# Kernel optimization log

Measured on AMD Instinct MI355X. Metric: run time of the kernel, lower is better.

The kernel has to match this reference:

```python
import jax, jax.numpy as jnp
import numpy as np

# ConvMem dims
B, Cx, Cy, L, K, S, N = 64, 16, 64, 32, 5, 1, 1024
M = (L - K) // S + 1  # 28
DT, TAU_X, TAU_Y = 0.1, 1.0, 0.1
ETA_X, ETA_Y = DT / TAU_X, DT / TAU_Y
MAX_STEPS = 50


def setup_inputs() -> dict:
    key = jax.random.key(0)
    k1, k2, k3, k4 = jax.random.split(key, 4)
    x0 = jax.random.normal(k1, (B, Cx, L, L), dtype=jnp.float32)
    f0 = jax.random.uniform(k2, (B, Cy, M, M), dtype=jnp.float32) / 100.0
    # Conv2d weight (shared between conv and convT), shape (Cy, Cx, K, K)
    w_conv = jax.random.normal(k3, (Cy, Cx, K, K), dtype=jnp.float32) / np.sqrt(Cx * K * K).astype(np.float32)
    # W: (N, Cy*M*M), kaiming_normal fan_in init
    W = jax.random.normal(k4, (N, Cy * M * M), dtype=jnp.float32) * np.sqrt(2.0 / (Cy * M * M)).astype(np.float32)
    return {"x0": x0, "f0": f0, "w_conv": w_conv, "W": W}


def _conv(x, w):
    # PyTorch Conv2d(Cx, Cy, K, S, bias=False), valid padding
    return jax.lax.conv_general_dilated(x, w, (S, S), 'VALID',
                                        dimension_numbers=('NCHW', 'OIHW', 'NCHW'))


def _convT(f, w):
    # PyTorch ConvTranspose2d with the *same* weight as conv (adjoint of _conv)
    return jax.lax.conv_transpose(f, w, (S, S), 'VALID',
                                  dimension_numbers=('NCHW', 'OIHW', 'NCHW'),
                                  transpose_kernel=True)


def reference(x0, f0, w_conv, W):
    def step(carry, _):
        x_prev, f_prev = carry
        # fc: z = W @ flatten(f_prev);  g = softmax(z) over N (dim=1, beta=1)
        z = jnp.einsum('nk,bk->bn', W, f_prev.reshape(B, Cy * M * M))  # (B, N)
        g = jax.nn.softmax(z, axis=1)
        # fcT: y = W^T @ g, reshaped to (B, Cy, M, M)
        y = (g @ W).reshape(B, Cy, M, M)
        # f nonlin: softmax over channel dim (dim=1)
        f_new = jax.nn.softmax(y + _conv(x_prev, w_conv), axis=1)
        x_new = _convT(f_prev, w_conv)
        f = (1.0 - ETA_Y) * f_prev + ETA_Y * f_new
        x = (1.0 - ETA_X) * x_prev + ETA_X * x_new
        return (x, f), None

    (x, f), _ = jax.lax.scan(step, (x0, f0), None, length=MAX_STEPS)
    return x, f
```

## Files before the change

kernel.cpp:

```cpp
#include <hip/hip_runtime.h>

#define BB 64
#define CXC 16
#define CYC 64
#define LL 32
#define MM 28
#define NN 1024
#define SP 784
#define KTOT 50176
#define NSTEPS 50
#define NSPLIT 49

using short8  = __attribute__((ext_vector_type(8))) short;
using floatx4 = __attribute__((ext_vector_type(4))) float;

typedef __attribute__((address_space(1))) unsigned int gu32;
typedef __attribute__((address_space(3))) unsigned int su32;

__device__ __forceinline__ ushort f2b(float v) {
    union { float f; unsigned u; } a; a.f = v;
    unsigned r = a.u + 0x7fff + ((a.u >> 16) & 1);
    return (ushort)(r >> 16);
}
__device__ __forceinline__ unsigned pk2(float a, float b) {
    return (unsigned)f2b(a) | ((unsigned)f2b(b) << 16);
}
__device__ __forceinline__ float b2f(ushort u) {
    union { unsigned u; float f; } a; a.u = ((unsigned)u) << 16; return a.f;
}

__device__ __forceinline__ unsigned char f2e4(float v) {
    const unsigned u = __float_as_uint(v);
    const unsigned s = (u >> 24) & 0x80;
    float a = fabsf(v);
    if (a >= 448.f) return (unsigned char)(s | 0x7E);
    if (a < 0.015625f) {
        int q = (int)rintf(a * 512.f);
        return (unsigned char)(s | (unsigned)q);
    }
    unsigned au = u & 0x7fffffffu;
    unsigned r = au + 0xFFFFFu + ((au >> 20) & 1u);
    int exp = (int)(r >> 23) - 127;
    if (exp > 8) return (unsigned char)(s | 0x7E);
    unsigned mant = (r >> 20) & 7u;
    return (unsigned char)(s | (((unsigned)(exp + 7)) << 3) | mant);
}

#define WSC 256.0f
#define FSC 64.0f
#define GSC 256.0f
#define ZDESC (1.0f / (WSC * FSC))
#define YDESC (1.0f / (WSC * GSC))

__global__ __launch_bounds__(256) void wconvert_kernel(const float* __restrict__ W,
                                                       unsigned char* __restrict__ Wb8,
                                                       unsigned char* __restrict__ WT8) {
    __shared__ float t[32][33];
    const int k0 = blockIdx.x * 32, n0 = blockIdx.y * 32;
    const int tid = threadIdx.x, r = tid >> 5, c = tid & 31;
#pragma unroll
    for (int p = 0; p < 4; p++) {
        const int rr = r + p * 8;
        t[rr][c] = W[(size_t)(n0 + rr) * KTOT + k0 + c];
    }
    __syncthreads();
    const int rw = tid >> 3, c4 = (tid & 7) * 4;
#if __has_builtin(__builtin_amdgcn_cvt_pk_fp8_f32)
    unsigned u1 = 0, u2 = 0;
    u1 = __builtin_amdgcn_cvt_pk_fp8_f32(t[rw][c4 + 0] * WSC, t[rw][c4 + 1] * WSC, u1, false);
    u1 = __builtin_amdgcn_cvt_pk_fp8_f32(t[rw][c4 + 2] * WSC, t[rw][c4 + 3] * WSC, u1, true);
    *(unsigned*)&Wb8[(size_t)(n0 + rw) * KTOT + k0 + c4] = u1;
    u2 = __builtin_amdgcn_cvt_pk_fp8_f32(t[c4 + 0][rw] * WSC, t[c4 + 1][rw] * WSC, u2, false);
    u2 = __builtin_amdgcn_cvt_pk_fp8_f32(t[c4 + 2][rw] * WSC, t[c4 + 3][rw] * WSC, u2, true);
    *(unsigned*)&WT8[(size_t)(k0 + rw) * NN + n0 + c4] = u2;
#else
    uchar4 o1, o2;
    o1.x = f2e4(t[rw][c4 + 0] * WSC); o1.y = f2e4(t[rw][c4 + 1] * WSC);
    o1.z = f2e4(t[rw][c4 + 2] * WSC); o1.w = f2e4(t[rw][c4 + 3] * WSC);
    *(uchar4*)&Wb8[(size_t)(n0 + rw) * KTOT + k0 + c4] = o1;
    o2.x = f2e4(t[c4 + 0][rw] * WSC); o2.y = f2e4(t[c4 + 1][rw] * WSC);
    o2.z = f2e4(t[c4 + 2][rw] * WSC); o2.w = f2e4(t[c4 + 3][rw] * WSC);
    *(uchar4*)&WT8[(size_t)(k0 + rw) * NN + n0 + c4] = o2;
#endif
}

__global__ __launch_bounds__(256) void cvt_f0_kernel(const float* __restrict__ f,
                                                     unsigned char* __restrict__ o) {
    const size_t i = ((size_t)blockIdx.x * 256 + threadIdx.x) * 4;
    const float4 v = *(const float4*)(f + i);
    uchar4 pk;
    pk.x = f2e4(v.x * FSC); pk.y = f2e4(v.y * FSC);
    pk.z = f2e4(v.z * FSC); pk.w = f2e4(v.w * FSC);
    *(uchar4*)(o + i) = pk;
}

__global__ __launch_bounds__(256) void wbuild_kernel(const float* __restrict__ wc,
                                                     ushort* __restrict__ wcA,
                                                     ushort* __restrict__ wcT) {
    const int bid = blockIdx.x, tid = threadIdx.x;
    if (bid < 64) {
        const int cy = bid;
        for (int k = tid; k < 416; k += 256) {
            const int tap = k >> 4, cx = k & 15;
            const float v = (tap < 25) ? wc[cy * 400 + cx * 25 + tap] : 0.f;
            wcA[cy * 416 + k] = f2b(v);
        }
    } else {
        const int cx = bid - 64;
        for (int k = tid; k < 1600; k += 256) {
            const int tap = k >> 6, cy = k & 63;
            wcT[cx * 1600 + k] = f2b(wc[cy * 400 + cx * 25 + tap]);
        }
    }
}

__global__ __launch_bounds__(256) void init_x_kernel(const float* __restrict__ x0,
                                                     float* __restrict__ xcl,
                                                     ushort* __restrict__ x16) {
    const int b = blockIdx.x, tid = threadIdx.x;
    __shared__ float xs[16384];
    for (int c = tid; c < 4096; c += 256)
        ((float4*)xs)[c] = ((const float4*)(x0 + (size_t)b * 16384))[c];
    __syncthreads();
    for (int p = tid; p < 1024; p += 256) {
        float v[16];
#pragma unroll
        for (int cx = 0; cx < 16; cx++) v[cx] = xs[cx * 1024 + p];
        float* dst = xcl + ((size_t)b * 1024 + p) * 16;
#pragma unroll
        for (int q = 0; q < 4; q++)
            *(float4*)(dst + q * 4) = make_float4(v[q*4], v[q*4+1], v[q*4+2], v[q*4+3]);
        uint4 u0, u1;
        u0.x = pk2(v[0], v[1]);  u0.y = pk2(v[2], v[3]);
        u0.z = pk2(v[4], v[5]);  u0.w = pk2(v[6], v[7]);
        u1.x = pk2(v[8], v[9]);  u1.y = pk2(v[10], v[11]);
        u1.z = pk2(v[12], v[13]); u1.w = pk2(v[14], v[15]);
        ushort* d16 = x16 + ((size_t)b * 1024 + p) * 16;
        *(uint4*)d16 = u0; *(uint4*)(d16 + 8) = u1;
    }
}

__global__ __launch_bounds__(256) void final_x_kernel(const float* __restrict__ xcl,
                                                      float* __restrict__ dout) {
    const int b = blockIdx.x, tid = threadIdx.x;
    __shared__ float xs[16384];
    for (int c = tid; c < 4096; c += 256)
        ((float4*)xs)[c] = ((const float4*)(xcl + (size_t)b * 16384))[c];
    __syncthreads();
    for (int idx = tid; idx < 16384; idx += 256) {
        const int cx = idx >> 10, p = idx & 1023;
        dout[(size_t)b * 16384 + idx] = xs[p * 16 + cx];
    }
}

__global__ __launch_bounds__(256) void init_fpad_kernel(const float* __restrict__ f0,
                                                        ushort* __restrict__ fpad) {
    const int b = blockIdx.x, rg = blockIdx.y;
    const int tid = threadIdx.x;
    __shared__ float fs[64 * 112];
    const float* src = f0 + (size_t)b * KTOT + rg * 112;
    for (int c = tid; c < 1792; c += 256) {
        const int cy = c / 28, p4 = (c % 28) * 4;
        *(float4*)&fs[cy * 112 + p4] = *(const float4*)(src + (size_t)cy * SP + p4);
    }
    __syncthreads();
    for (int c = tid; c < 896; c += 256) {
        const int pl = c >> 3, g8 = (c & 7) * 8;
        union { ushort u[8]; uint4 v; } pk;
#pragma unroll
        for (int e = 0; e < 8; e++) pk.u[e] = f2b(fs[(g8 + e) * 112 + pl]);
        const int pos = rg * 112 + pl, i = pos / 28, j = pos % 28;
        *(uint4*)(fpad + (((size_t)b * 36 + 4 + i) * 36 + 4 + j) * 64 + g8) = pk.v;
    }
}

__global__ __launch_bounds__(256, 3) void gemm1_kernel(const unsigned char* __restrict__ A,
                                                       const unsigned char* __restrict__ B,
                                                       float* __restrict__ C) {
    const int bx = blockIdx.x, by = blockIdx.y;
    const int tid = threadIdx.x, l = tid & 63, w = tid >> 6;
    const int wr = w >> 1, wc = w & 1;
    const int lr = l & 15, lg = l >> 4;
    const int sw = (lr >> 1) & 3;
    const int hi8 = (lg & 1) * 8;
    __shared__ __attribute__((aligned(16))) unsigned char As[2][4096];
    __shared__ __attribute__((aligned(16))) unsigned char Bs[2][8192];

    floatx4 acc[2][4];
#pragma unroll
    for (int mi = 0; mi < 2; mi++)
#pragma unroll
        for (int ni = 0; ni < 4; ni++) acc[mi][ni] = (floatx4){0.f, 0.f, 0.f, 0.f};

    const size_t kbase = (size_t)by * 1024;

    auto STAGE = [&](int buf, int kc) {
        const size_t koff = kbase + (size_t)kc * 64;
        {
            const int row = tid >> 2;
            const int kk = (((tid & 3) ^ ((row >> 1) & 3)) << 4);
            __builtin_amdgcn_global_load_lds((gu32*)(A + (size_t)row * KTOT + koff + kk),
                                             (su32*)&As[buf][tid * 16], 16, 0, 0);
        }
#pragma unroll
        for (int i = 0; i < 2; i++) {
            const int q = i * 256 + tid;
            const int rl = q >> 2;
            const int kk = (((q & 3) ^ ((rl >> 1) & 3)) << 4);
            const int row = bx * 128 + rl;
            __builtin_amdgcn_global_load_lds((gu32*)(B + (size_t)row * KTOT + koff + kk),
                                             (su32*)&Bs[buf][q * 16], 16, 0, 0);
        }
    };

    STAGE(0, 0);
#pragma unroll 1
    for (int kc = 0; kc < 16; kc++) {
        const int cur = kc & 1;
        if (kc < 15) {
            STAGE(cur ^ 1, kc + 1);
            asm volatile("s_waitcnt vmcnt(3)" ::: "memory");
        } else {
            asm volatile("s_waitcnt vmcnt(0)" ::: "memory");
        }
        __builtin_amdgcn_s_barrier();
#pragma unroll
        for (int kb = 0; kb < 2; kb++) {
            const int co = (((kb * 2 + (lg >> 1)) ^ sw) << 4) + hi8;
            long a[2];
#pragma unroll
            for (int mi = 0; mi < 2; mi++)
                a[mi] = *(const long*)&As[cur][(wr * 32 + mi * 16 + lr) * 64 + co];
#pragma unroll
            for (int ni = 0; ni < 4; ni++) {
                const long b = *(const long*)&Bs[cur][(wc * 64 + ni * 16 + lr) * 64 + co];
                acc[0][ni] = __builtin_amdgcn_mfma_f32_16x16x32_fp8_fp8(a[0], b, acc[0][ni], 0, 0, 0);
                acc[1][ni] = __builtin_amdgcn_mfma_f32_16x16x32_fp8_fp8(a[1], b, acc[1][ni], 0, 0, 0);
            }
        }
        __builtin_amdgcn_s_barrier();
    }
    float* cp = C + (size_t)by * (BB * NN) + (size_t)(wr * 32 + ((l >> 4) << 2)) * NN
              + bx * 128 + wc * 64 + (l & 15);
#pragma unroll
    for (int mi = 0; mi < 2; mi++)
#pragma unroll
        for (int ni = 0; ni < 4; ni++)
#pragma unroll
            for (int q = 0; q < 4; q++)
                cp[(size_t)(mi * 16 + q) * NN + ni * 16] = acc[mi][ni][q];
}

__global__ __launch_bounds__(1024) void softmax_g_kernel(const float* __restrict__ zpart,
                                                         unsigned char* __restrict__ g8) {
    const int b = blockIdx.x, tid = threadIdx.x;
    float s = 0.f;
#pragma unroll 7
    for (int sp = 0; sp < NSPLIT; sp++) s += zpart[(size_t)sp * (BB * NN) + b * NN + tid];
    s *= ZDESC;
    __shared__ float red[32];
    float m = s;
#pragma unroll
    for (int off = 32; off > 0; off >>= 1) m = fmaxf(m, __shfl_down(m, off));
    if ((tid & 63) == 0) red[tid >> 6] = m;
    __syncthreads();
    float bm = red[0];
#pragma unroll
    for (int e = 1; e < 16; e++) bm = fmaxf(bm, red[e]);
    const float ev = __expf(s - bm);
    float ssum = ev;
#pragma unroll
    for (int off = 32; off > 0; off >>= 1) ssum += __shfl_down(ssum, off);
    __syncthreads();
    if ((tid & 63) == 0) red[16 + (tid >> 6)] = ssum;
    __syncthreads();
    float tot = red[16];
#pragma unroll
    for (int e = 1; e < 16; e++) tot += red[16 + e];
    g8[b * NN + tid] = f2e4(ev * (GSC / tot));
}

__global__ __launch_bounds__(256, 3) void gemm2_convT_kernel(const unsigned char* __restrict__ A,
                                                             const unsigned char* __restrict__ B,
                                                             float* __restrict__ C,
                                                             const ushort* __restrict__ fpad,
                                                             const ushort* __restrict__ wcT,
                                                             const float* __restrict__ xin,
                                                             float* __restrict__ xout,
                                                             ushort* __restrict__ x16o) {
    __shared__ __attribute__((aligned(16))) unsigned char As[2][4096];
    __shared__ __attribute__((aligned(16))) unsigned char Bs[2][8192];
    const int tid = threadIdx.x, l = tid & 63, w = tid >> 6;
    const int lr = l & 15, lg = l >> 4;

    if (blockIdx.x < 256) {
        const int sub = blockIdx.x, b = sub & 63, pg = sub >> 6;
        floatx4 acc[4];
#pragma unroll
        for (int n = 0; n < 4; n++) acc[n] = (floatx4){0.f, 0.f, 0.f, 0.f};
        int p[4], p1[4], p2[4];
#pragma unroll
        for (int n = 0; n < 4; n++) {
            p[n]  = pg * 256 + (w * 4 + n) * 16 + lr;
            p1[n] = p[n] >> 5;
            p2[n] = p[n] & 31;
        }
        const ushort* fb_b = fpad + (size_t)b * (36 * 36 * 64);
        const int cy_lo = lg * 8;

        for (int s = 0; s < 50; s++) {
            const short8 af = *(const short8*)(wcT + (size_t)lr * 1600 + s * 32 + lg * 8);
            const int tap = s >> 1;
            const int ky = tap / 5, kx = tap % 5;
            const int cy_lane = ((s & 1) << 5) + cy_lo;
            short8 bf[4];
#pragma unroll
            for (int n = 0; n < 4; n++) {
                const size_t ad = (((size_t)(p1[n] + 4 - ky)) * 36 + (p2[n] + 4 - kx)) * 64 + cy_lane;
                bf[n] = *(const short8*)(fb_b + ad);
            }
#pragma unroll
            for (int n = 0; n < 4; n++)
                acc[n] = __builtin_amdgcn_mfma_f32_16x16x32_bf16(af, bf[n], acc[n], 0, 0, 0);
        }
#pragma unroll
        for (int n = 0; n < 4; n++) {
            const size_t base = ((size_t)b * 1024 + p[n]) * 16 + lg * 4;
            const float4 xo = *(const float4*)(xin + base);
            float4 r;
            r.x = 0.9f * xo.x + 0.1f * acc[n][0];
            r.y = 0.9f * xo.y + 0.1f * acc[n][1];
            r.z = 0.9f * xo.z + 0.1f * acc[n][2];
            r.w = 0.9f * xo.w + 0.1f * acc[n][3];
            *(float4*)(xout + base) = r;
            uint2 pk; pk.x = pk2(r.x, r.y); pk.y = pk2(r.z, r.w);
            *(uint2*)(x16o + base) = pk;
        }
        return;
    }

    const int bx = blockIdx.x - 256;
    const int wr = w >> 1, wc = w & 1;
    const int sw = (lr >> 1) & 3;
    const int hi8 = (lg & 1) * 8;

    floatx4 acc[2][4];
#pragma unroll
    for (int mi = 0; mi < 2; mi++)
#pragma unroll
        for (int ni = 0; ni < 4; ni++) acc[mi][ni] = (floatx4){0.f, 0.f, 0.f, 0.f};

    auto STAGE = [&](int buf, int kc) {
        const size_t koff = (size_t)kc * 64;
        {
            const int row = tid >> 2;
            const int kk = (((tid & 3) ^ ((row >> 1) & 3)) << 4);
            __builtin_amdgcn_global_load_lds((gu32*)(A + (size_t)row * NN + koff + kk),
                                             (su32*)&As[buf][tid * 16], 16, 0, 0);
        }
#pragma unroll
        for (int i = 0; i < 2; i++) {
            const int q = i * 256 + tid;
            const int rl = q >> 2;
            const int kk = (((q & 3) ^ ((rl >> 1) & 3)) << 4);
            const int row = bx * 128 + rl;
            __builtin_amdgcn_global_load_lds((gu32*)(B + (size_t)row * NN + koff + kk),
                                             (su32*)&Bs[buf][q * 16], 16, 0, 0);
        }
    };

    STAGE(0, 0);
#pragma unroll 1
    for (int kc = 0; kc < 16; kc++) {
        const int cur = kc & 1;
        if (kc < 15) {
            STAGE(cur ^ 1, kc + 1);
            asm volatile("s_waitcnt vmcnt(3)" ::: "memory");
        } else {
            asm volatile("s_waitcnt vmcnt(0)" ::: "memory");
        }
        __builtin_amdgcn_s_barrier();
#pragma unroll
        for (int kb = 0; kb < 2; kb++) {
            const int co = (((kb * 2 + (lg >> 1)) ^ sw) << 4) + hi8;
            long a[2];
#pragma unroll
            for (int mi = 0; mi < 2; mi++)
                a[mi] = *(const long*)&As[cur][(wr * 32 + mi * 16 + lr) * 64 + co];
#pragma unroll
            for (int ni = 0; ni < 4; ni++) {
                const long b = *(const long*)&Bs[cur][(wc * 64 + ni * 16 + lr) * 64 + co];
                acc[0][ni] = __builtin_amdgcn_mfma_f32_16x16x32_fp8_fp8(a[0], b, acc[0][ni], 0, 0, 0);
                acc[1][ni] = __builtin_amdgcn_mfma_f32_16x16x32_fp8_fp8(a[1], b, acc[1][ni], 0, 0, 0);
            }
        }
        __builtin_amdgcn_s_barrier();
    }
    float* cp = C + (size_t)(wr * 32 + ((l >> 4) << 2)) * KTOT
              + bx * 128 + wc * 64 + (l & 15);
#pragma unroll
    for (int mi = 0; mi < 2; mi++)
#pragma unroll
        for (int ni = 0; ni < 4; ni++)
#pragma unroll
            for (int q = 0; q < 4; q++)
                cp[(size_t)(mi * 16 + q) * KTOT + ni * 16] = acc[mi][ni][q];
}

__global__ __launch_bounds__(256) void conv_mfma_kernel(const ushort* __restrict__ x16,
                                                        const ushort* __restrict__ wcA,
                                                        const float* __restrict__ y,
                                                        ushort* __restrict__ fpad,
                                                        unsigned char* __restrict__ f8std,
                                                        float* __restrict__ f32o,
                                                        const int write_f) {
    const int b = blockIdx.x, rg = blockIdx.y;
    const int tid = threadIdx.x, l = tid & 63, w = tid >> 6;
    const int lr = l & 15, lg = l >> 4;
    __shared__ float yt[64 * 196];
    ushort* ft = (ushort*)yt;

    {
        const float* yb = y + (size_t)b * KTOT + rg * 196;
        for (int c = tid; c < 3136; c += 256) {
            const int cy = c / 49, p4 = (c % 49) * 4;
            float4 v = *(const float4*)(yb + (size_t)cy * SP + p4);
            v.x *= YDESC; v.y *= YDESC; v.z *= YDESC; v.w *= YDESC;
            *(float4*)&yt[cy * 196 + p4] = v;
        }
    }

    const int nf = (w == 0) ? 4 : 3;
    const int fb = (w == 0) ? 0 : (1 + 3 * w);

    floatx4 acc[4][4];
#pragma unroll
    for (int m = 0; m < 4; m++)
#pragma unroll
        for (int n = 0; n < 4; n++) acc[m][n] = (floatx4){0.f, 0.f, 0.f, 0.f};

    int pos_l[4], ii[4], jj[4];
#pragma unroll
    for (int n = 0; n < 4; n++) {
        int pl = (fb + n) * 16 + lr;
        if (pl > 195) pl = 195;
        pos_l[n] = pl;
        ii[n] = rg * 7 + pl / 28;
        jj[n] = pl % 28;
    }

    const int t_lane = lg >> 1;
    const int cx0 = (lg & 1) * 8;
    const ushort* xb = x16 + ((size_t)b << 14);

    for (int s = 0; s < 13; s++) {
        short8 af[4];
#pragma unroll
        for (int m = 0; m < 4; m++)
            af[m] = *(const short8*)(wcA + (size_t)(m * 16 + lr) * 416 + s * 32 + lg * 8);
        const int tap = 2 * s + t_lane;
        const int ky = tap / 5, kx = tap % 5;
        short8 bf[4];
#pragma unroll
        for (int n = 0; n < 4; n++) {
            if (n < nf) {
                const int pp = (ii[n] + ky) * 32 + (jj[n] + kx);
                bf[n] = *(const short8*)(xb + (size_t)pp * 16 + cx0);
            }
        }
#pragma unroll
        for (int n = 0; n < 4; n++) {
            if (n < nf) {
#pragma unroll
                for (int m = 0; m < 4; m++)
                    acc[m][n] = __builtin_amdgcn_mfma_f32_16x16x32_bf16(af[m], bf[n], acc[m][n], 0, 0, 0);
            }
        }
    }
    __syncthreads();

#pragma unroll
    for (int n = 0; n < 4; n++) {
        if (n < nf) {
            float v[16];
#pragma unroll
            for (int m = 0; m < 4; m++)
#pragma unroll
                for (int q = 0; q < 4; q++) {
                    const int cy = m * 16 + lg * 4 + q;
                    v[m * 4 + q] = acc[m][n][q] + yt[cy * 196 + pos_l[n]];
                }
            float mx = v[0];
#pragma unroll
            for (int e = 1; e < 16; e++) mx = fmaxf(mx, v[e]);
            mx = fmaxf(mx, __shfl_xor(mx, 16));
            mx = fmaxf(mx, __shfl_xor(mx, 32));
            float ss = 0.f;
#pragma unroll
            for (int e = 0; e < 16; e++) { v[e] = __expf(v[e] - mx); ss += v[e]; }
            ss += __shfl_xor(ss, 16);
            ss += __shfl_xor(ss, 32);
            const float inv = 1.0f / ss;
            const bool valid = (((fb + n) * 16 + lr) < 196) && write_f;
            float* fo = f32o + (size_t)b * KTOT + rg * 196 + pos_l[n];
#pragma unroll
            for (int m = 0; m < 4; m++)
#pragma unroll
                for (int q = 0; q < 4; q++) {
                    const int cy = m * 16 + lg * 4 + q;
                    const float fv = v[m * 4 + q] * inv;
                    acc[m][n][q] = fv;
                    if (valid) fo[(size_t)cy * SP] = fv;
                }
        }
    }
    __syncthreads();

#pragma unroll
    for (int n = 0; n < 4; n++) {
        if (n < nf) {
#pragma unroll
            for (int m = 0; m < 4; m++)
#pragma unroll
                for (int q = 0; q < 4; q++)
                    ft[pos_l[n] * 72 + m * 16 + lg * 4 + q] = f2b(acc[m][n][q]);
        }
    }
    __syncthreads();

    for (int c = tid; c < 196 * 4; c += 256) {
        const int pl = c >> 2, ch = (c & 3) * 16;
        const uint4 v0 = *(const uint4*)&ft[pl * 72 + ch];
        const uint4 v1 = *(const uint4*)&ft[pl * 72 + ch + 8];
        const int gi = rg * 7 + pl / 28, gj = pl % 28;
        ushort* dst = fpad + (((size_t)b * 36 + 4 + gi) * 36 + 4 + gj) * 64 + ch;
        *(uint4*)dst = v0; *(uint4*)(dst + 8) = v1;
    }
    for (int c = tid; c < 1600; c += 256) {
        const int cy = c & 63, p8 = (c >> 6) * 8;
        if (p8 < 196) {
            union { unsigned char u[8]; unsigned w[2]; } pk;
#pragma unroll
            for (int e = 0; e < 8; e++)
                pk.u[e] = f2e4(b2f(ft[(p8 + e) * 72 + cy]) * FSC);
            unsigned* dst = (unsigned*)(f8std + (size_t)b * KTOT + (size_t)cy * SP + rg * 196 + p8);
            dst[0] = pk.w[0];
            if (p8 <= 188) dst[1] = pk.w[1];
        }
    }
}

extern "C" void kernel_launch(void* const* d_in, const int* in_sizes, int n_in,
                              void* d_out, int out_size, void* d_ws, size_t ws_size,
                              hipStream_t stream) {
    const float* x0    = (const float*)d_in[0];
    const float* f0    = (const float*)d_in[1];
    const float* wconv = (const float*)d_in[2];
    const float* W     = (const float*)d_in[3];

    const size_t XSZ = (size_t)BB * CXC * LL * LL;
    const size_t FSZ = (size_t)BB * KTOT;

    char* pp = (char*)d_ws;
    unsigned char* Wb8  = (unsigned char*)pp; pp += (size_t)NN * KTOT;
    unsigned char* WT8  = (unsigned char*)pp; pp += (size_t)NN * KTOT;
    float*  xcl0  = (float*)pp;  pp += (size_t)BB * 1024 * 16 * 4;
    float*  xcl1  = (float*)pp;  pp += (size_t)BB * 1024 * 16 * 4;
    ushort* x16a  = (ushort*)pp; pp += (size_t)BB * 1024 * 16 * 2;
    ushort* x16b  = (ushort*)pp; pp += (size_t)BB * 1024 * 16 * 2;
    pp += 4096;
    ushort* fpad  = (ushort*)pp; pp += (size_t)BB * 36 * 36 * 64 * 2;
    unsigned char* f8std = (unsigned char*)pp; pp += FSZ;
    float*  zy    = (float*)pp;  pp += (size_t)NSPLIT * BB * NN * 4;
    unsigned char* g8 = (unsigned char*)pp; pp += (size_t)BB * NN;
    ushort* wcA   = (ushort*)pp; pp += (size_t)64 * 416 * 2;
    ushort* wcT   = (ushort*)pp; pp += (size_t)16 * 1600 * 2;

    float*  xcl[2] = {xcl0, xcl1};
    ushort* x16[2] = {x16a, x16b};
    float*  f32o = (float*)d_out + XSZ;

    hipMemsetAsync(fpad, 0, (size_t)BB * 36 * 36 * 64 * 2, stream);
    hipMemsetAsync(x16a, 0, (size_t)BB * 1024 * 16 * 2 * 2 + 4096, stream);

    wconvert_kernel<<<dim3(KTOT / 32, NN / 32), 256, 0, stream>>>(W, Wb8, WT8);
    wbuild_kernel<<<80, 256, 0, stream>>>(wconv, wcA, wcT);
    init_x_kernel<<<64, 256, 0, stream>>>(x0, xcl0, x16a);
    cvt_f0_kernel<<<(int)(FSZ / 1024), 256, 0, stream>>>(f0, f8std);
    init_fpad_kernel<<<dim3(64, 7), 256, 0, stream>>>(f0, fpad);

    for (int t = 0; t < NSTEPS; t++) {
        const int cur = t & 1, nxt = cur ^ 1;
        gemm1_kernel<<<dim3(8, NSPLIT), 256, 0, stream>>>(f8std, Wb8, zy);
        softmax_g_kernel<<<BB, 1024, 0, stream>>>(zy, g8);
        gemm2_convT_kernel<<<256 + KTOT / 128, 256, 0, stream>>>(
            g8, WT8, zy, fpad, wcT, xcl[cur], xcl[nxt], x16[nxt]);
        conv_mfma_kernel<<<dim3(64, 4), 256, 0, stream>>>(x16[cur], wcA, zy, fpad, f8std, f32o,
                                                          t == NSTEPS - 1 ? 1 : 0);
    }
    final_x_kernel<<<64, 256, 0, stream>>>(xcl[0], (float*)d_out);
}
```

Measured before the change: 4.338 ms.

## Triple-buffer GEMM LDS stages and widen W conversion tiles

Both fp8 GEMM kernels move from double to triple LDS buffering. This lets the trailing barrier in each k-iteration be dropped, since a buffer is only overwritten two stages later. The W fp8 conversion/transpose kernel now uses 64x64 tiles with float4 loads and 16-byte packed stores instead of 32x32 tiles with scalar traffic. The cost is more LDS per block (36KB instead of 24KB), which may reduce occupancy. Removing the barrier also depends on the single remaining barrier being enough to order reads against later async writes.

```diff
diff --git a/kernel.cpp b/kernel.cpp
--- a/kernel.cpp
+++ b/kernel.cpp
@@ -46,6 +46,18 @@
     return (unsigned char)(s | (((unsigned)(exp + 7)) << 3) | mant);
 }
 
+__device__ __forceinline__ unsigned pk4e4(float a, float b, float c, float d) {
+#if __has_builtin(__builtin_amdgcn_cvt_pk_fp8_f32)
+    unsigned u = 0;
+    u = __builtin_amdgcn_cvt_pk_fp8_f32(a, b, u, false);
+    u = __builtin_amdgcn_cvt_pk_fp8_f32(c, d, u, true);
+    return u;
+#else
+    return (unsigned)f2e4(a) | ((unsigned)f2e4(b) << 8)
+         | ((unsigned)f2e4(c) << 16) | ((unsigned)f2e4(d) << 24);
+#endif
+}
+
 #define WSC 256.0f
 #define FSC 64.0f
 #define GSC 256.0f
@@ -55,33 +67,34 @@
 __global__ __launch_bounds__(256) void wconvert_kernel(const float* __restrict__ W,
                                                        unsigned char* __restrict__ Wb8,
                                                        unsigned char* __restrict__ WT8) {
-    __shared__ float t[32][33];
-    const int k0 = blockIdx.x * 32, n0 = blockIdx.y * 32;
-    const int tid = threadIdx.x, r = tid >> 5, c = tid & 31;
-#pragma unroll
-    for (int p = 0; p < 4; p++) {
-        const int rr = r + p * 8;
-        t[rr][c] = W[(size_t)(n0 + rr) * KTOT + k0 + c];
-    }
-    __syncthreads();
-    const int rw = tid >> 3, c4 = (tid & 7) * 4;
-#if __has_builtin(__builtin_amdgcn_cvt_pk_fp8_f32)
-    unsigned u1 = 0, u2 = 0;
-    u1 = __builtin_amdgcn_cvt_pk_fp8_f32(t[rw][c4 + 0] * WSC, t[rw][c4 + 1] * WSC, u1, false);
-    u1 = __builtin_amdgcn_cvt_pk_fp8_f32(t[rw][c4 + 2] * WSC, t[rw][c4 + 3] * WSC, u1, true);
-    *(unsigned*)&Wb8[(size_t)(n0 + rw) * KTOT + k0 + c4] = u1;
-    u2 = __builtin_amdgcn_cvt_pk_fp8_f32(t[c4 + 0][rw] * WSC, t[c4 + 1][rw] * WSC, u2, false);
-    u2 = __builtin_amdgcn_cvt_pk_fp8_f32(t[c4 + 2][rw] * WSC, t[c4 + 3][rw] * WSC, u2, true);
-    *(unsigned*)&WT8[(size_t)(k0 + rw) * NN + n0 + c4] = u2;
-#else
-    uchar4 o1, o2;
-    o1.x = f2e4(t[rw][c4 + 0] * WSC); o1.y = f2e4(t[rw][c4 + 1] * WSC);
-    o1.z = f2e4(t[rw][c4 + 2] * WSC); o1.w = f2e4(t[rw][c4 + 3] * WSC);
-    *(uchar4*)&Wb8[(size_t)(n0 + rw) * KTOT + k0 + c4] = o1;
-    o2.x = f2e4(t[c4 + 0][rw] * WSC); o2.y = f2e4(t[c4 + 1][rw] * WSC);
-    o2.z = f2e4(t[c4 + 2][rw] * WSC); o2.w = f2e4(t[c4 + 3][rw] * WSC);
-    *(uchar4*)&WT8[(size_t)(k0 + rw) * NN + n0 + c4] = o2;
-#endif
+    __shared__ float t[64 * 68];
+    const int k0 = blockIdx.x * 64, n0 = blockIdx.y * 64;
+    const int tid = threadIdx.x;
+    for (int c = tid; c < 1024; c += 256) {
+        const int row = c >> 4, col4 = (c & 15) * 4;
+        const float4 v = *(const float4*)(W + (size_t)(n0 + row) * KTOT + k0 + col4);
+        *(float4*)&t[row * 68 + col4] = v;
+    }
+    __syncthreads();
+    const int rr = tid >> 2, cb = (tid & 3) * 16;
+    {
+        uint4 o;
+        const float* p = &t[rr * 68 + cb];
+        o.x = pk4e4(p[0] * WSC,  p[1] * WSC,  p[2] * WSC,  p[3] * WSC);
+        o.y = pk4e4(p[4] * WSC,  p[5] * WSC,  p[6] * WSC,  p[7] * WSC);
+        o.z = pk4e4(p[8] * WSC,  p[9] * WSC,  p[10] * WSC, p[11] * WSC);
+        o.w = pk4e4(p[12] * WSC, p[13] * WSC, p[14] * WSC, p[15] * WSC);
+        *(uint4*)&Wb8[(size_t)(n0 + rr) * KTOT + k0 + cb] = o;
+    }
+    {
+        uint4 o;
+        const float* p = &t[cb * 68 + rr];
+        o.x = pk4e4(p[0*68] * WSC,  p[1*68] * WSC,  p[2*68] * WSC,  p[3*68] * WSC);
+        o.y = pk4e4(p[4*68] * WSC,  p[5*68] * WSC,  p[6*68] * WSC,  p[7*68] * WSC);
+        o.z = pk4e4(p[8*68] * WSC,  p[9*68] * WSC,  p[10*68] * WSC, p[11*68] * WSC);
+        o.w = pk4e4(p[12*68] * WSC, p[13*68] * WSC, p[14*68] * WSC, p[15*68] * WSC);
+        *(uint4*)&WT8[(size_t)(k0 + rr) * NN + n0 + cb] = o;
+    }
 }
 
 __global__ __launch_bounds__(256) void cvt_f0_kernel(const float* __restrict__ f,
@@ -183,8 +196,8 @@
     const int lr = l & 15, lg = l >> 4;
     const int sw = (lr >> 1) & 3;
     const int hi8 = (lg & 1) * 8;
-    __shared__ __attribute__((aligned(16))) unsigned char As[2][4096];
-    __shared__ __attribute__((aligned(16))) unsigned char Bs[2][8192];
+    __shared__ __attribute__((aligned(16))) unsigned char As[3 * 4096];
+    __shared__ __attribute__((aligned(16))) unsigned char Bs[3 * 8192];
 
     floatx4 acc[2][4];
 #pragma unroll
@@ -200,7 +213,7 @@
             const int row = tid >> 2;
             const int kk = (((tid & 3) ^ ((row >> 1) & 3)) << 4);
             __builtin_amdgcn_global_load_lds((gu32*)(A + (size_t)row * KTOT + koff + kk),
-                                             (su32*)&As[buf][tid * 16], 16, 0, 0);
+                                             (su32*)&As[buf * 4096 + tid * 16], 16, 0, 0);
         }
 #pragma unroll
         for (int i = 0; i < 2; i++) {
@@ -209,16 +222,17 @@
             const int kk = (((q & 3) ^ ((rl >> 1) & 3)) << 4);
             const int row = bx * 128 + rl;
             __builtin_amdgcn_global_load_lds((gu32*)(B + (size_t)row * KTOT + koff + kk),
-                                             (su32*)&Bs[buf][q * 16], 16, 0, 0);
+                                             (su32*)&Bs[buf * 8192 + q * 16], 16, 0, 0);
         }
     };
 
     STAGE(0, 0);
+    int cur = 0;
 #pragma unroll 1
     for (int kc = 0; kc < 16; kc++) {
-        const int cur = kc & 1;
         if (kc < 15) {
-            STAGE(cur ^ 1, kc + 1);
+            int nb = cur + 1; if (nb == 3) nb = 0;
+            STAGE(nb, kc + 1);
             asm volatile("s_waitcnt vmcnt(3)" ::: "memory");
         } else {
             asm volatile("s_waitcnt vmcnt(0)" ::: "memory");
@@ -230,15 +244,15 @@
             long a[2];
 #pragma unroll
             for (int mi = 0; mi < 2; mi++)
-                a[mi] = *(const long*)&As[cur][(wr * 32 + mi * 16 + lr) * 64 + co];
+                a[mi] = *(const long*)&As[cur * 4096 + (wr * 32 + mi * 16 + lr) * 64 + co];
 #pragma unroll
             for (int ni = 0; ni < 4; ni++) {
-                const long b = *(const long*)&Bs[cur][(wc * 64 + ni * 16 + lr) * 64 + co];
+                const long b = *(const long*)&Bs[cur * 8192 + (wc * 64 + ni * 16 + lr) * 64 + co];
                 acc[0][ni] = __builtin_amdgcn_mfma_f32_16x16x32_fp8_fp8(a[0], b, acc[0][ni], 0, 0, 0);
                 acc[1][ni] = __builtin_amdgcn_mfma_f32_16x16x32_fp8_fp8(a[1], b, acc[1][ni], 0, 0, 0);
             }
         }
-        __builtin_amdgcn_s_barrier();
+        cur = cur + 1; if (cur == 3) cur = 0;
     }
     float* cp = C + (size_t)by * (BB * NN) + (size_t)(wr * 32 + ((l >> 4) << 2)) * NN
               + bx * 128 + wc * 64 + (l & 15);
@@ -288,8 +302,8 @@
                                                              const float* __restrict__ xin,
                                                              float* __restrict__ xout,
                                                              ushort* __restrict__ x16o) {
-    __shared__ __attribute__((aligned(16))) unsigned char As[2][4096];
-    __shared__ __attribute__((aligned(16))) unsigned char Bs[2][8192];
+    __shared__ __attribute__((aligned(16))) unsigned char As[3 * 4096];
+    __shared__ __attribute__((aligned(16))) unsigned char Bs[3 * 8192];
     const int tid = threadIdx.x, l = tid & 63, w = tid >> 6;
     const int lr = l & 15, lg = l >> 4;
 
@@ -356,7 +370,7 @@
             const int row = tid >> 2;
             const int kk = (((tid & 3) ^ ((row >> 1) & 3)) << 4);
             __builtin_amdgcn_global_load_lds((gu32*)(A + (size_t)row * NN + koff + kk),
-                                             (su32*)&As[buf][tid * 16], 16, 0, 0);
+                                             (su32*)&As[buf * 4096 + tid * 16], 16, 0, 0);
         }
 #pragma unroll
         for (int i = 0; i < 2; i++) {
@@ -365,16 +379,17 @@
             const int kk = (((q & 3) ^ ((rl >> 1) & 3)) << 4);
             const int row = bx * 128 + rl;
             __builtin_amdgcn_global_load_lds((gu32*)(B + (size_t)row * NN + koff + kk),
-                                             (su32*)&Bs[buf][q * 16], 16, 0, 0);
+                                             (su32*)&Bs[buf * 8192 + q * 16], 16, 0, 0);
         }
     };
 
     STAGE(0, 0);
+    int cur = 0;
 #pragma unroll 1
     for (int kc = 0; kc < 16; kc++) {
-        const int cur = kc & 1;
         if (kc < 15) {
-            STAGE(cur ^ 1, kc + 1);
+            int nb = cur + 1; if (nb == 3) nb = 0;
+            STAGE(nb, kc + 1);
             asm volatile("s_waitcnt vmcnt(3)" ::: "memory");
         } else {
             asm volatile("s_waitcnt vmcnt(0)" ::: "memory");
@@ -386,15 +401,15 @@
             long a[2];
 #pragma unroll
             for (int mi = 0; mi < 2; mi++)
-                a[mi] = *(const long*)&As[cur][(wr * 32 + mi * 16 + lr) * 64 + co];
+                a[mi] = *(const long*)&As[cur * 4096 + (wr * 32 + mi * 16 + lr) * 64 + co];
 #pragma unroll
             for (int ni = 0; ni < 4; ni++) {
-                const long b = *(const long*)&Bs[cur][(wc * 64 + ni * 16 + lr) * 64 + co];
+                const long b = *(const long*)&Bs[cur * 8192 + (wc * 64 + ni * 16 + lr) * 64 + co];
                 acc[0][ni] = __builtin_amdgcn_mfma_f32_16x16x32_fp8_fp8(a[0], b, acc[0][ni], 0, 0, 0);
                 acc[1][ni] = __builtin_amdgcn_mfma_f32_16x16x32_fp8_fp8(a[1], b, acc[1][ni], 0, 0, 0);
             }
         }
-        __builtin_amdgcn_s_barrier();
+        cur = cur + 1; if (cur == 3) cur = 0;
     }
     float* cp = C + (size_t)(wr * 32 + ((l >> 4) << 2)) * KTOT
               + bx * 128 + wc * 64 + (l & 15);
@@ -583,7 +598,7 @@
     hipMemsetAsync(fpad, 0, (size_t)BB * 36 * 36 * 64 * 2, stream);
     hipMemsetAsync(x16a, 0, (size_t)BB * 1024 * 16 * 2 * 2 + 4096, stream);
 
-    wconvert_kernel<<<dim3(KTOT / 32, NN / 32), 256, 0, stream>>>(W, Wb8, WT8);
+    wconvert_kernel<<<dim3(KTOT / 64, NN / 64), 256, 0, stream>>>(W, Wb8, WT8);
     wbuild_kernel<<<80, 256, 0, stream>>>(wconv, wcA, wcT);
     init_x_kernel<<<64, 256, 0, stream>>>(x0, xcl0, x16a);
     cvt_f0_kernel<<<(int)(FSZ / 1024), 256, 0, stream>>>(f0, f8std);
```

Result: no change. 4.275 ms (-1.5%).
